# Kernel tuning notes

Measured on AMD Instinct MI355X. Metric: run time of the kernel, lower is better.

Reference implementation:

```python
import jax, jax.numpy as jnp
import numpy as np

B, S, D, H = 4, 1500, 1280, 20
HD = D // H  # 64

def setup_inputs() -> dict:
    key = jax.random.key(0)
    ks = jax.random.split(key, 8)
    scale = 1.0 / np.sqrt(D)
    return {
        "hidden_states": jax.random.normal(ks[0], (B, S, D), dtype=jnp.float32),
        "attention_mask": jnp.zeros((B, 1, S, S), dtype=jnp.float32),
        "q_w": jax.random.normal(ks[1], (D, D), dtype=jnp.float32) * scale,
        "q_b": jax.random.normal(ks[2], (D,), dtype=jnp.float32) * 0.02,
        "k_w": jax.random.normal(ks[3], (D, D), dtype=jnp.float32) * scale,
        "v_w": jax.random.normal(ks[4], (D, D), dtype=jnp.float32) * scale,
        "v_b": jax.random.normal(ks[5], (D,), dtype=jnp.float32) * 0.02,
        "o_w": jax.random.normal(ks[6], (D, D), dtype=jnp.float32) * scale,
        "o_b": jax.random.normal(ks[7], (D,), dtype=jnp.float32) * 0.02,
    }

def reference(hidden_states, attention_mask, q_w, q_b, k_w, v_w, v_b, o_w, o_b):
    bsz, seq_len, d_model = hidden_states.shape
    scaling = HD ** (-0.5)
    # Projections (k_proj has NO bias, matching the module)
    q = hidden_states @ q_w + q_b
    k = hidden_states @ k_w
    v = hidden_states @ v_w + v_b
    # [B, H, S, HD]
    q = q.reshape(bsz, seq_len, H, HD).transpose(0, 2, 1, 3)
    k = k.reshape(bsz, seq_len, H, HD).transpose(0, 2, 1, 3)
    v = v.reshape(bsz, seq_len, H, HD).transpose(0, 2, 1, 3)
    scores = jnp.einsum("bhqd,bhkd->bhqk", q, k) * scaling
    scores = scores + attention_mask
    attn = jax.nn.softmax(scores.astype(jnp.float32), axis=-1).astype(q.dtype)
    out = jnp.einsum("bhqk,bhkd->bhqd", attn, v)
    out = out.transpose(0, 2, 1, 3).reshape(bsz, seq_len, d_model)
    return out @ o_w + o_b
```

## Files before the change

### kernel.cpp

```cpp
#include <hip/hip_runtime.h>
#include <hip/hip_bf16.h>
#include <cstddef>

#define B_   4
#define S_   1500
#define D_   1280
#define H_   20
#define HD_  64
#define M_   (B_*S_)
#define SPAD 1536
#define BIGNEG (-1e30f)
#define LOG2E 1.44269504088896340736f
#define KVB  64
#define NTA  24

typedef short bf16x8 __attribute__((ext_vector_type(8)));
typedef float f32x4 __attribute__((ext_vector_type(4)));
typedef unsigned short u16;
typedef u16 u16x8 __attribute__((ext_vector_type(8)));
typedef unsigned int u32x4v __attribute__((ext_vector_type(4)));

#define MFMA __builtin_amdgcn_mfma_f32_16x16x32_bf16

__device__ __forceinline__ u16 f2bf(float f) {
  union { float f; unsigned u; } x; x.f = f;
  unsigned r = (x.u + 0x7fffu + ((x.u >> 16) & 1u)) >> 16;
  return (u16)r;
}

__device__ __forceinline__ unsigned cvtpk(float a, float b) {
  unsigned r;
  asm volatile("v_cvt_pk_bf16_f32 %0, %1, %2" : "=v"(r) : "v"(a), "v"(b));
  return r;
}

__device__ __forceinline__ void gl_lds16(const u16* g, u16* l) {
  typedef __attribute__((address_space(1))) const unsigned GU;
  typedef __attribute__((address_space(3))) unsigned LU;
  __builtin_amdgcn_global_load_lds((GU*)g, (LU*)l, 16, 0, 0);
}

__global__ __launch_bounds__(256) void k_conv(const float* __restrict__ X, u16* __restrict__ Y) {
  size_t i = (size_t)blockIdx.x * 256 + threadIdx.x;
  const float4* p = (const float4*)(X + i * 8);
  float4 a = p[0], b = p[1];
  u16x8 v;
  v[0]=f2bf(a.x); v[1]=f2bf(a.y); v[2]=f2bf(a.z); v[3]=f2bf(a.w);
  v[4]=f2bf(b.x); v[5]=f2bf(b.y); v[6]=f2bf(b.z); v[7]=f2bf(b.w);
  *(u16x8*)(Y + i * 8) = v;
}

__global__ __launch_bounds__(256) void k_mscan(const float* __restrict__ m, int* __restrict__ flag) {
  const size_t tot = (size_t)B_ * S_ * S_;
  size_t i = ((size_t)blockIdx.x * 256 + threadIdx.x) * 4;
  size_t stride = (size_t)gridDim.x * 256 * 4;
  for (; i < tot; i += stride) {
    float4 v = *(const float4*)(m + i);
    if (v.x != 0.f || v.y != 0.f || v.z != 0.f || v.w != 0.f) {
      int b = (int)(i / ((size_t)S_ * S_));
      atomicOr(&flag[b], 1);
    }
  }
}

__global__ __launch_bounds__(256) void k_trans4(const float* __restrict__ qw,
                                                const float* __restrict__ kw,
                                                const float* __restrict__ vw,
                                                const float* __restrict__ ow,
                                                u16* __restrict__ Wt) {
  const float* W = (blockIdx.z == 0) ? qw : (blockIdx.z == 1) ? kw
                   : (blockIdx.z == 2) ? vw : ow;
  u16* dst = Wt + (size_t)blockIdx.z * D_ * D_;
  __shared__ float t[32][33];
  int n0 = blockIdx.x * 32, k0 = blockIdx.y * 32;
  int tx = threadIdx.x & 31, ty = threadIdx.x >> 5;
  #pragma unroll
  for (int i = ty; i < 32; i += 8) t[i][tx] = W[(size_t)(k0 + i) * D_ + n0 + tx];
  __syncthreads();
  #pragma unroll
  for (int i = ty; i < 32; i += 8) dst[(size_t)(n0 + i) * D_ + k0 + tx] = f2bf(t[tx][i]);
}

__global__ __launch_bounds__(256) void k_vtrans(const u16* __restrict__ Vb, u16* __restrict__ Vt) {
  __shared__ u16 t[128][72];
  int bh = blockIdx.x, b = bh / H_, h = bh % H_;
  int s0 = blockIdx.y * 128;
  int tid = threadIdx.x;
  #pragma unroll
  for (int r = 0; r < 4; r++) {
    int sl = r * 32 + (tid >> 3);
    int s = s0 + sl; if (s > S_ - 1) s = S_ - 1;
    bf16x8 v = *(const bf16x8*)(Vb + ((size_t)(b * S_ + s)) * D_ + h * HD_ + (tid & 7) * 8);
    *(bf16x8*)&t[sl][(tid & 7) * 8] = v;
  }
  __syncthreads();
  #pragma unroll
  for (int r = 0; r < 4; r++) {
    int d = r * 16 + (tid >> 4);
    int ss = (tid & 15) * 8;
    u16x8 o;
    #pragma unroll
    for (int q = 0; q < 8; q++) {
      int sl = ss + q;
      int kk = ((sl >> 4) & 3) * 4 + (sl & 3) + ((sl >> 2) & 3) * 16 + (sl & 64);
      o[q] = t[kk][d];
    }
    *(u16x8*)(Vt + ((size_t)bh * HD_ + d) * SPAD + s0 + ss) = o;
  }
}

__global__ __launch_bounds__(256) void k_gemmqkv(const u16* __restrict__ A,
                                                 const u16* __restrict__ Wt,
                                                 const float* __restrict__ q_b,
                                                 const float* __restrict__ v_b,
                                                 u16* __restrict__ Qb) {
  int p = blockIdx.x;
  int gg = p & 7;
  int idx = p >> 3;
  int y = idx / 6;
  int x = gg * 6 + idx % 6;
  if (x >= 47) return;

  __shared__ u16 As[2][128 * 64];
  __shared__ u16 Bs[2][128 * 64];
  int tid = threadIdx.x;
  int lane = tid & 63;
  int wv = tid >> 6;
  int l16 = lane & 15, lg = lane >> 4;
  int wr = wv >> 1, wc = wv & 1;
  int m0 = x * 128;
  int n0g = y * 128;
  int sel = y / 10;
  int nloc = n0g - sel * 1280;

  int srow = tid >> 3;
  int csw = ((tid & 7) ^ (srow & 7)) * 8;
  const u16* asrc = A + csw;
  const u16* bsrc = Wt + csw;
  int dbase = wv * 8 * 64;

  f32x4 acc[4][4] = {};

#define STAGEG(tt, bufb) do {                                            \
    int kk0 = (tt) * 64;                                                 \
    _Pragma("unroll")                                                    \
    for (int c = 0; c < 4; c++) {                                        \
      int row = srow + c * 32;                                           \
      int ar = m0 + row; if (ar > M_ - 1) ar = M_ - 1;                   \
      gl_lds16(asrc + (size_t)ar * D_ + kk0,                             \
               &As[bufb][0] + dbase + c * 2048);                         \
      gl_lds16(bsrc + (size_t)(n0g + row) * D_ + kk0,                    \
               &Bs[bufb][0] + dbase + c * 2048);                         \
    }                                                                    \
  } while (0)

  STAGEG(0, 0);
  __syncthreads();
  for (int t = 0; t < 20; t++) {
    int cb = t & 1;
    if (t < 19) STAGEG(t + 1, cb ^ 1);
    const u16* AsC = &As[cb][0];
    const u16* BsC = &Bs[cb][0];
    #pragma unroll
    for (int kk = 0; kk < 2; kk++) {
      int pcol = ((kk * 4 + lg) ^ (l16 & 7)) * 8;
      bf16x8 af[4], bf[4];
      #pragma unroll
      for (int m = 0; m < 4; m++)
        af[m] = *(const bf16x8*)&AsC[(wr * 64 + m * 16 + l16) * 64 + pcol];
      #pragma unroll
      for (int n = 0; n < 4; n++)
        bf[n] = *(const bf16x8*)&BsC[(wc * 64 + n * 16 + l16) * 64 + pcol];
      __builtin_amdgcn_s_setprio(1);
      #pragma unroll
      for (int m = 0; m < 4; m++)
        #pragma unroll
        for (int n = 0; n < 4; n++)
          acc[m][n] = MFMA(af[m], bf[n], acc[m][n], 0, 0, 0);
      __builtin_amdgcn_s_setprio(0);
    }
    __syncthreads();
  }
#undef STAGEG

  const float* bias = (sel == 0) ? q_b : v_b;
  float scl = (sel == 0) ? (0.125f * LOG2E) : 1.0f;
  u16* outb = Qb + (size_t)sel * ((size_t)M_ * D_);

  #pragma unroll
  for (int m = 0; m < 4; m++) {
    int row0 = m0 + wr * 64 + m * 16 + lg * 4;
    #pragma unroll
    for (int n = 0; n < 4; n++) {
      int colL = nloc + wc * 64 + n * 16 + l16;
      float bv = (sel == 1) ? 0.0f : bias[colL];
      #pragma unroll
      for (int j = 0; j < 4; j++) {
        int row = row0 + j;
        if (row < M_) {
          float v = (acc[m][n][j] + bv) * scl;
          outb[(size_t)row * D_ + colL] = f2bf(v);
        }
      }
    }
  }
}

__global__ __launch_bounds__(256) void k_gemmo(const u16* __restrict__ A,
                                               const u16* __restrict__ Wt,
                                               const float* __restrict__ bias,
                                               float* __restrict__ outp) {
  int p = blockIdx.x;
  int gg = p & 7;
  int idx = p >> 3;
  int y = idx / 6;
  int x = gg * 6 + idx % 6;
  if (x >= 47) return;

  __shared__ u16 As[2][128 * 64];
  __shared__ u16 Bs[2][128 * 64];
  int tid = threadIdx.x;
  int lane = tid & 63;
  int wv = tid >> 6;
  int l16 = lane & 15, lg = lane >> 4;
  int wr = wv >> 1, wc = wv & 1;
  int m0 = x * 128, n0 = y * 128;

  int srow = tid >> 3;
  int csw = ((tid & 7) ^ (srow & 7)) * 8;
  const u16* asrc = A + csw;
  const u16* bsrc = Wt + csw;
  int dbase = wv * 8 * 64;

  f32x4 acc[4][4] = {};

#define STAGEG(tt, bufb) do {                                            \
    int kk0 = (tt) * 64;                                                 \
    _Pragma("unroll")                                                    \
    for (int c = 0; c < 4; c++) {                                        \
      int row = srow + c * 32;                                           \
      int ar = m0 + row; if (ar > M_ - 1) ar = M_ - 1;                   \
      gl_lds16(asrc + (size_t)ar * D_ + kk0,                             \
               &As[bufb][0] + dbase + c * 2048);                         \
      gl_lds16(bsrc + (size_t)(n0 + row) * D_ + kk0,                     \
               &Bs[bufb][0] + dbase + c * 2048);                         \
    }                                                                    \
  } while (0)

  STAGEG(0, 0);
  __syncthreads();
  for (int t = 0; t < 20; t++) {
    int cb = t & 1;
    if (t < 19) STAGEG(t + 1, cb ^ 1);
    const u16* AsC = &As[cb][0];
    const u16* BsC = &Bs[cb][0];
    #pragma unroll
    for (int kk = 0; kk < 2; kk++) {
      int pcol = ((kk * 4 + lg) ^ (l16 & 7)) * 8;
      bf16x8 af[4], bf[4];
      #pragma unroll
      for (int m = 0; m < 4; m++)
        af[m] = *(const bf16x8*)&AsC[(wr * 64 + m * 16 + l16) * 64 + pcol];
      #pragma unroll
      for (int n = 0; n < 4; n++)
        bf[n] = *(const bf16x8*)&BsC[(wc * 64 + n * 16 + l16) * 64 + pcol];
      __builtin_amdgcn_s_setprio(1);
      #pragma unroll
      for (int m = 0; m < 4; m++)
        #pragma unroll
        for (int n = 0; n < 4; n++)
          acc[m][n] = MFMA(af[m], bf[n], acc[m][n], 0, 0, 0);
      __builtin_amdgcn_s_setprio(0);
    }
    __syncthreads();
  }
#undef STAGEG

  #pragma unroll
  for (int m = 0; m < 4; m++) {
    int row0 = m0 + wr * 64 + m * 16 + lg * 4;
    #pragma unroll
    for (int n = 0; n < 4; n++) {
      int col = n0 + wc * 64 + n * 16 + l16;
      float bv = bias[col];
      #pragma unroll
      for (int j = 0; j < 4; j++) {
        int row = row0 + j;
        if (row < M_) outp[(size_t)row * D_ + col] = acc[m][n][j] + bv;
      }
    }
  }
}

__global__ __launch_bounds__(256) void k_attn(const u16* __restrict__ Qb,
                                              const u16* __restrict__ Kb,
                                              const u16* __restrict__ Vt,
                                              const float* __restrict__ mask,
                                              const int* __restrict__ mflag,
                                              u16* __restrict__ Ctx) {
  __shared__ u16 Kl[2][64 * 64];
  __shared__ u16 Vl[2][64 * 64];

  int p = blockIdx.x;
  int L = (p & 7) * 120 + (p >> 3);
  int h = L % 20;
  int g = L / 20;
  int b = g / 12;
  int xq = g % 12;
  int bh = b * H_ + h;
  int um = mflag[b];

  int tid = threadIdx.x;
  int lane = tid & 63, wv = tid >> 6;
  int l16 = lane & 15, lg = lane >> 4;
  int qw0 = xq * 128 + wv * 16;

  int qr0 = qw0 + l16;      if (qr0 > S_ - 1) qr0 = S_ - 1;
  int qr1 = qw0 + 64 + l16; if (qr1 > S_ - 1) qr1 = S_ - 1;
  const u16* qp0 = Qb + ((size_t)(b * S_ + qr0)) * D_ + h * HD_ + lg * 8;
  const u16* qp1 = Qb + ((size_t)(b * S_ + qr1)) * D_ + h * HD_ + lg * 8;
  bf16x8 aq00 = *(const bf16x8*)(qp0);
  bf16x8 aq01 = *(const bf16x8*)(qp0 + 32);
  bf16x8 aq10 = *(const bf16x8*)(qp1);
  bf16x8 aq11 = *(const bf16x8*)(qp1 + 32);
  const float* mrow0 = mask + (size_t)b * S_ * S_ + (size_t)qr0 * S_;
  const float* mrow1 = mask + (size_t)b * S_ * S_ + (size_t)qr1 * S_;

  int sr0 = wv * 16 + (lane >> 3);
  int csw = ((lane & 7) ^ (lane >> 3)) * 8;
  const u16* ksrc = Kb + (size_t)b * S_ * D_ + h * HD_ + csw;
  const u16* vsrc0 = Vt + ((size_t)bh * HD_ + sr0) * SPAD + csw;
  const u16* vsrc1 = vsrc0 + 8 * SPAD;

  float m0_ = BIGNEG, l0_ = 0.0f, m1_ = BIGNEG, l1_ = 0.0f;
  f32x4 acc0[4] = {}, acc1[4] = {};
  const f32x4 zf = {0, 0, 0, 0};
  float4 mvA[4], mvB[4];
  #pragma unroll
  for (int sub = 0; sub < 4; sub++) { mvA[sub] = make_float4(0,0,0,0); mvB[sub] = make_float4(0,0,0,0); }

#define STAGE(k0s, bufb) do {                                          \
    int key0_ = (k0s) + sr0;     if (key0_ > S_ - 1) key0_ = S_ - 1;   \
    int key1_ = key0_ + 8;       if (key1_ > S_ - 1) key1_ = S_ - 1;   \
    u16* kd_ = &Kl[bufb][0] + wv * 1024;                               \
    u16* vd_ = &Vl[bufb][0] + wv * 1024;                               \
    gl_lds16(ksrc + (size_t)key0_ * D_, kd_);                          \
    gl_lds16(ksrc + (size_t)key1_ * D_, kd_ + 512);                    \
    gl_lds16(vsrc0 + (k0s), vd_);                                      \
    gl_lds16(vsrc1 + (k0s), vd_ + 512);                                \
  } while (0)

#define SMX(sv, mm, ll, accv) do {                                     \
    float t0 = fmaxf(fmaxf(sv[0][0], sv[0][1]), fmaxf(sv[0][2], sv[0][3])); \
    float t1 = fmaxf(fmaxf(sv[1][0], sv[1][1]), fmaxf(sv[1][2], sv[1][3])); \
    float t2 = fmaxf(fmaxf(sv[2][0], sv[2][1]), fmaxf(sv[2][2], sv[2][3])); \
    float t3 = fmaxf(fmaxf(sv[3][0], sv[3][1]), fmaxf(sv[3][2], sv[3][3])); \
    float rmax = fmaxf(fmaxf(t0, t1), fmaxf(t2, t3));                  \
    rmax = fmaxf(rmax, __shfl_xor(rmax, 16));                          \
    rmax = fmaxf(rmax, __shfl_xor(rmax, 32));                          \
    float mn = fmaxf(mm, rmax);                                        \
    if (!__all(mn - mm <= 8.0f)) {                                     \
      float c = __builtin_amdgcn_exp2f(mm - mn);                       \
      mm = mn; ll *= c;                                                \
      _Pragma("unroll")                                                \
      for (int j = 0; j < 4; j++) {                                    \
        float cj = __shfl(c, lg * 4 + j);                              \
        accv[0][j] *= cj; accv[1][j] *= cj;                            \
        accv[2][j] *= cj; accv[3][j] *= cj;                            \
      }                                                                \
    }                                                                  \
    _Pragma("unroll")                                                  \
    for (int sub = 0; sub < 4; sub++)                                  \
      _Pragma("unroll")                                                \
      for (int j = 0; j < 4; j++)                                      \
        sv[sub][j] = __builtin_amdgcn_exp2f(sv[sub][j] - mm);          \
    float a0 = (sv[0][0] + sv[0][1]) + (sv[0][2] + sv[0][3]);          \
    float a1 = (sv[1][0] + sv[1][1]) + (sv[1][2] + sv[1][3]);          \
    float a2 = (sv[2][0] + sv[2][1]) + (sv[2][2] + sv[2][3]);          \
    float a3 = (sv[3][0] + sv[3][1]) + (sv[3][2] + sv[3][3]);          \
    float rs = (a0 + a1) + (a2 + a3);                                  \
    rs += __shfl_xor(rs, 16);                                          \
    rs += __shfl_xor(rs, 32);                                          \
    ll += rs;                                                          \
  } while (0)

#define COMPUTE(curb, k0_, LASTV) do {                                 \
    const u16* KlC = &Kl[curb][0];                                     \
    const u16* VlC = &Vl[curb][0];                                     \
    f32x4 s0[4], s1[4];                                                \
    __builtin_amdgcn_s_setprio(1);                                     \
    _Pragma("unroll")                                                  \
    for (int sub = 0; sub < 4; sub++) {                                \
      const u16* kb = KlC + (sub * 16 + l16) * 64;                     \
      bf16x8 kf0 = *(const bf16x8*)(kb + ((lg     ^ (l16 & 7)) * 8));  \
      bf16x8 kf1 = *(const bf16x8*)(kb + (((4+lg) ^ (l16 & 7)) * 8));  \
      s0[sub] = MFMA(kf0, aq00, zf, 0, 0, 0);                          \
      s0[sub] = MFMA(kf1, aq01, s0[sub], 0, 0, 0);                     \
      s1[sub] = MFMA(kf0, aq10, zf, 0, 0, 0);                          \
      s1[sub] = MFMA(kf1, aq11, s1[sub], 0, 0, 0);                     \
    }                                                                  \
    __builtin_amdgcn_s_setprio(0);                                     \
    if (um) {                                                          \
      _Pragma("unroll")                                                \
      for (int sub = 0; sub < 4; sub++) {                              \
        s0[sub][0] = fmaf(mvA[sub].x, LOG2E, s0[sub][0]);              \
        s0[sub][1] = fmaf(mvA[sub].y, LOG2E, s0[sub][1]);              \
        s0[sub][2] = fmaf(mvA[sub].z, LOG2E, s0[sub][2]);              \
        s0[sub][3] = fmaf(mvA[sub].w, LOG2E, s0[sub][3]);              \
        s1[sub][0] = fmaf(mvB[sub].x, LOG2E, s1[sub][0]);              \
        s1[sub][1] = fmaf(mvB[sub].y, LOG2E, s1[sub][1]);              \
        s1[sub][2] = fmaf(mvB[sub].z, LOG2E, s1[sub][2]);              \
        s1[sub][3] = fmaf(mvB[sub].w, LOG2E, s1[sub][3]);              \
      }                                                                \
    }                                                                  \
    if (LASTV) {                                                       \
      _Pragma("unroll")                                                \
      for (int sub = 0; sub < 4; sub++) {                              \
        int kb_ = (k0_) + sub * 16 + lg * 4;                           \
        _Pragma("unroll")                                              \
        for (int j = 0; j < 4; j++)                                    \
          if (kb_ + j >= S_) { s0[sub][j] = BIGNEG; s1[sub][j] = BIGNEG; } \
      }                                                                \
    }                                                                  \
    SMX(s0, m0_, l0_, acc0);                                           \
    union { u32x4v u; bf16x8 bf; } pA0, pA1;                           \
    pA0.u[0] = cvtpk(s0[0][0], s0[0][1]); pA0.u[1] = cvtpk(s0[0][2], s0[0][3]); \
    pA0.u[2] = cvtpk(s0[1][0], s0[1][1]); pA0.u[3] = cvtpk(s0[1][2], s0[1][3]); \
    pA1.u[0] = cvtpk(s0[2][0], s0[2][1]); pA1.u[1] = cvtpk(s0[2][2], s0[2][3]); \
    pA1.u[2] = cvtpk(s0[3][0], s0[3][1]); pA1.u[3] = cvtpk(s0[3][2], s0[3][3]); \
    SMX(s1, m1_, l1_, acc1);                                           \
    union { u32x4v u; bf16x8 bf; } pB0, pB1;                           \
    pB0.u[0] = cvtpk(s1[0][0], s1[0][1]); pB0.u[1] = cvtpk(s1[0][2], s1[0][3]); \
    pB0.u[2] = cvtpk(s1[1][0], s1[1][1]); pB0.u[3] = cvtpk(s1[1][2], s1[1][3]); \
    pB1.u[0] = cvtpk(s1[2][0], s1[2][1]); pB1.u[1] = cvtpk(s1[2][2], s1[2][3]); \
    pB1.u[2] = cvtpk(s1[3][0], s1[3][1]); pB1.u[3] = cvtpk(s1[3][2], s1[3][3]); \
    __builtin_amdgcn_s_setprio(1);                                     \
    _Pragma("unroll")                                                  \
    for (int n = 0; n < 4; n++) {                                      \
      const u16* vb = VlC + (n * 16 + l16) * 64;                       \
      bf16x8 bv0 = *(const bf16x8*)(vb + (((lg*2  ) ^ (l16 & 7)) * 8));\
      bf16x8 bv1 = *(const bf16x8*)(vb + (((lg*2+1) ^ (l16 & 7)) * 8));\
      acc0[n] = MFMA(pA0.bf, bv0, acc0[n], 0, 0, 0);                   \
      acc0[n] = MFMA(pA1.bf, bv1, acc0[n], 0, 0, 0);                   \
      acc1[n] = MFMA(pB0.bf, bv0, acc1[n], 0, 0, 0);                   \
      acc1[n] = MFMA(pB1.bf, bv1, acc1[n], 0, 0, 0);                   \
    }                                                                  \
    __builtin_amdgcn_s_setprio(0);                                     \
  } while (0)

  STAGE(0, 0);
  if (um) {
    #pragma unroll
    for (int sub = 0; sub < 4; sub++) {
      mvA[sub] = *(const float4*)(mrow0 + sub * 16 + lg * 4);
      mvB[sub] = *(const float4*)(mrow1 + sub * 16 + lg * 4);
    }
  }
  asm volatile("" ::: "memory");

  for (int t = 0; t < NTA - 1; t++) {
    int k0 = t * KVB;
    int k1 = k0 + KVB;
    __builtin_amdgcn_s_barrier();
    asm volatile("" ::: "memory");
    STAGE(k1, (t + 1) & 1);
    float4 nA[4], nB[4];
    if (um) {
      #pragma unroll
      for (int sub = 0; sub < 4; sub++) {
        int mc = k1 + sub * 16 + lg * 4; if (mc > S_ - 4) mc = S_ - 4;
        nA[sub] = *(const float4*)(mrow0 + mc);
        nB[sub] = *(const float4*)(mrow1 + mc);
      }
      asm volatile("s_waitcnt vmcnt(12)" ::: "memory");
    } else {
      asm volatile("s_waitcnt vmcnt(4)" ::: "memory");
    }
    __builtin_amdgcn_s_barrier();
    asm volatile("" ::: "memory");
    COMPUTE(t & 1, k0, false);
    if (um) {
      #pragma unroll
      for (int sub = 0; sub < 4; sub++) { mvA[sub] = nA[sub]; mvB[sub] = nB[sub]; }
    }
  }
  {
    const int k0 = (NTA - 1) * KVB;
    __builtin_amdgcn_s_barrier();
    if (um) asm volatile("s_waitcnt vmcnt(8)" ::: "memory");
    else    asm volatile("s_waitcnt vmcnt(0)" ::: "memory");
    __builtin_amdgcn_s_barrier();
    asm volatile("" ::: "memory");
    COMPUTE((NTA - 1) & 1, k0, true);
  }

  float inv0 = 1.0f / l0_;
  float inv1 = 1.0f / l1_;
  #pragma unroll
  for (int j = 0; j < 4; j++) {
    float ivj0 = __shfl(inv0, lg * 4 + j);
    float ivj1 = __shfl(inv1, lg * 4 + j);
    int row0 = qw0 + lg * 4 + j;
    int row1 = row0 + 64;
    if (row0 < S_) {
      #pragma unroll
      for (int n = 0; n < 4; n++)
        Ctx[((size_t)(b * S_ + row0)) * D_ + h * HD_ + n * 16 + l16] = f2bf(acc0[n][j] * ivj0);
    }
    if (row1 < S_) {
      #pragma unroll
      for (int n = 0; n < 4; n++)
        Ctx[((size_t)(b * S_ + row1)) * D_ + h * HD_ + n * 16 + l16] = f2bf(acc1[n][j] * ivj1);
    }
  }
#undef STAGE
#undef SMX
#undef COMPUTE
}

extern "C" void kernel_launch(void* const* d_in, const int* in_sizes, int n_in,
                              void* d_out, int out_size, void* d_ws, size_t ws_size,
                              hipStream_t stream) {
  const float* hs   = (const float*)d_in[0];
  const float* mask = (const float*)d_in[1];
  const float* q_w  = (const float*)d_in[2];
  const float* q_b  = (const float*)d_in[3];
  const float* k_w  = (const float*)d_in[4];
  const float* v_w  = (const float*)d_in[5];
  const float* v_b  = (const float*)d_in[6];
  const float* o_w  = (const float*)d_in[7];
  const float* o_b  = (const float*)d_in[8];
  float* out = (float*)d_out;

  char* w = (char*)d_ws;
  const size_t XD = (size_t)M_ * D_;
  const size_t WD = (size_t)D_ * D_;
  u16* Xb  = (u16*)(w);                 w += XD * 2;
  u16* Wtq = (u16*)(w);                 w += WD * 2;
  u16* Wtk = (u16*)(w);                 w += WD * 2;
  u16* Wtv = (u16*)(w);                 w += WD * 2;
  u16* Wto = (u16*)(w);                 w += WD * 2;
  u16* Qb  = (u16*)(w);                 w += XD * 2;
  u16* Kb  = (u16*)(w);                 w += XD * 2;
  u16* Vb  = (u16*)(w);                 w += XD * 2;
  u16* Vt  = (u16*)(w);                 w += (size_t)B_ * H_ * HD_ * SPAD * 2;
  int* mflag = (int*)(w);               w += 4 * sizeof(int);
  u16* Ctx = Xb;
  (void)Wtk; (void)Wtv;

  hipMemsetAsync(mflag, 0, 4 * sizeof(int), stream);
  k_mscan<<<dim3(2048), dim3(256), 0, stream>>>(mask, mflag);

  k_conv<<<dim3(3750), dim3(256), 0, stream>>>(hs, Xb);
  k_trans4<<<dim3(40, 40, 4), dim3(256), 0, stream>>>(q_w, k_w, v_w, o_w, Wtq);

  k_gemmqkv<<<dim3(1440), dim3(256), 0, stream>>>(Xb, Wtq, q_b, v_b, Qb);
  k_vtrans<<<dim3(80, 12), dim3(256), 0, stream>>>(Vb, Vt);

  k_attn<<<dim3(960), dim3(256), 0, stream>>>(Qb, Kb, Vt, mask, mflag, Ctx);

  k_gemmo<<<dim3(480), dim3(256), 0, stream>>>(Ctx, Wto, o_b, out);
}
```

Measured before the change: 253.1 us.

## Defer softmax row-sum reduction to epilogue and load mask inline

Drops the per-tile cross-lane shuffle reduction of the softmax denominator. Each lane now keeps a partial sum and the partials are combined once after the key loop, which is valid because every lane's partial is rescaled by the same row-max correction. The mask is no longer prefetched one tile ahead in registers. It is loaded directly inside the compute step, which lowers register pressure and simplifies the vmcnt waits. The cost is exposed global-load latency on the mask path when the mask is in use.

```diff
diff --git a/kernel.cpp b/kernel.cpp
--- a/kernel.cpp
+++ b/kernel.cpp
@@ -335,9 +335,6 @@
   float m0_ = BIGNEG, l0_ = 0.0f, m1_ = BIGNEG, l1_ = 0.0f;
   f32x4 acc0[4] = {}, acc1[4] = {};
   const f32x4 zf = {0, 0, 0, 0};
-  float4 mvA[4], mvB[4];
-  #pragma unroll
-  for (int sub = 0; sub < 4; sub++) { mvA[sub] = make_float4(0,0,0,0); mvB[sub] = make_float4(0,0,0,0); }
 
 #define STAGE(k0s, bufb) do {                                          \
     int key0_ = (k0s) + sr0;     if (key0_ > S_ - 1) key0_ = S_ - 1;   \
@@ -378,10 +375,7 @@
     float a1 = (sv[1][0] + sv[1][1]) + (sv[1][2] + sv[1][3]);          \
     float a2 = (sv[2][0] + sv[2][1]) + (sv[2][2] + sv[2][3]);          \
     float a3 = (sv[3][0] + sv[3][1]) + (sv[3][2] + sv[3][3]);          \
-    float rs = (a0 + a1) + (a2 + a3);                                  \
-    rs += __shfl_xor(rs, 16);                                          \
-    rs += __shfl_xor(rs, 32);                                          \
-    ll += rs;                                                          \
+    ll += (a0 + a1) + (a2 + a3);                                       \
   } while (0)
 
 #define COMPUTE(curb, k0_, LASTV) do {                                 \
@@ -400,17 +394,21 @@
       s1[sub] = MFMA(kf1, aq11, s1[sub], 0, 0, 0);                     \
     }                                                                  \
     __builtin_amdgcn_s_setprio(0);                                     \
-    if (um) {                                                          \
+    if (um) {   \
       _Pragma("unroll")                                                \
       for (int sub = 0; sub < 4; sub++) {                              \
-        s0[sub][0] = fmaf(mvA[sub].x, LOG2E, s0[sub][0]);              \
-        s0[sub][1] = fmaf(mvA[sub].y, LOG2E, s0[sub][1]);              \
-        s0[sub][2] = fmaf(mvA[sub].z, LOG2E, s0[sub][2]);              \
-        s0[sub][3] = fmaf(mvA[sub].w, LOG2E, s0[sub][3]);              \
-        s1[sub][0] = fmaf(mvB[sub].x, LOG2E, s1[sub][0]);              \
-        s1[sub][1] = fmaf(mvB[sub].y, LOG2E, s1[sub][1]);              \
-        s1[sub][2] = fmaf(mvB[sub].z, LOG2E, s1[sub][2]);              \
-        s1[sub][3] = fmaf(mvB[sub].w, LOG2E, s1[sub][3]);              \
+        int mc = (k0_) + sub * 16 + lg * 4;                            \
+        if (mc > S_ - 4) mc = S_ - 4;                                  \
+        float4 mv0 = *(const float4*)(mrow0 + mc);                     \
+        float4 mv1 = *(const float4*)(mrow1 + mc);                     \
+        s0[sub][0] = fmaf(mv0.x, LOG2E, s0[sub][0]);                   \
+        s0[sub][1] = fmaf(mv0.y, LOG2E, s0[sub][1]);                   \
+        s0[sub][2] = fmaf(mv0.z, LOG2E, s0[sub][2]);                   \
+        s0[sub][3] = fmaf(mv0.w, LOG2E, s0[sub][3]);                   \
+        s1[sub][0] = fmaf(mv1.x, LOG2E, s1[sub][0]);                   \
+        s1[sub][1] = fmaf(mv1.y, LOG2E, s1[sub][1]);                   \
+        s1[sub][2] = fmaf(mv1.z, LOG2E, s1[sub][2]);                   \
+        s1[sub][3] = fmaf(mv1.w, LOG2E, s1[sub][3]);                   \
       }                                                                \
     }                                                                  \
     if (LASTV) {                                                       \
@@ -449,51 +447,30 @@
   } while (0)
 
   STAGE(0, 0);
-  if (um) {
-    #pragma unroll
-    for (int sub = 0; sub < 4; sub++) {
-      mvA[sub] = *(const float4*)(mrow0 + sub * 16 + lg * 4);
-      mvB[sub] = *(const float4*)(mrow1 + sub * 16 + lg * 4);
-    }
-  }
-  asm volatile("" ::: "memory");
 
   for (int t = 0; t < NTA - 1; t++) {
     int k0 = t * KVB;
-    int k1 = k0 + KVB;
     __builtin_amdgcn_s_barrier();
     asm volatile("" ::: "memory");
-    STAGE(k1, (t + 1) & 1);
-    float4 nA[4], nB[4];
-    if (um) {
-      #pragma unroll
-      for (int sub = 0; sub < 4; sub++) {
-        int mc = k1 + sub * 16 + lg * 4; if (mc > S_ - 4) mc = S_ - 4;
-        nA[sub] = *(const float4*)(mrow0 + mc);
-        nB[sub] = *(const float4*)(mrow1 + mc);
-      }
-      asm volatile("s_waitcnt vmcnt(12)" ::: "memory");
-    } else {
-      asm volatile("s_waitcnt vmcnt(4)" ::: "memory");
-    }
+    STAGE(k0 + KVB, (t + 1) & 1);
+    asm volatile("s_waitcnt vmcnt(4)" ::: "memory");
     __builtin_amdgcn_s_barrier();
     asm volatile("" ::: "memory");
     COMPUTE(t & 1, k0, false);
-    if (um) {
-      #pragma unroll
-      for (int sub = 0; sub < 4; sub++) { mvA[sub] = nA[sub]; mvB[sub] = nB[sub]; }
-    }
   }
   {
     const int k0 = (NTA - 1) * KVB;
     __builtin_amdgcn_s_barrier();
-    if (um) asm volatile("s_waitcnt vmcnt(8)" ::: "memory");
-    else    asm volatile("s_waitcnt vmcnt(0)" ::: "memory");
+    asm volatile("s_waitcnt vmcnt(0)" ::: "memory");
     __builtin_amdgcn_s_barrier();
     asm volatile("" ::: "memory");
     COMPUTE((NTA - 1) & 1, k0, true);
   }
 
+  l0_ += __shfl_xor(l0_, 16);
+  l0_ += __shfl_xor(l0_, 32);
+  l1_ += __shfl_xor(l1_, 16);
+  l1_ += __shfl_xor(l1_, 32);
   float inv0 = 1.0f / l0_;
   float inv1 = 1.0f / l1_;
   #pragma unroll
```

After: 244.4 us. 1.04x faster.
